# Kernel tuning notes

Hardware: AMD Instinct MI355X
Metric: run time of the kernel (lower is better)

The kernel has to match this reference:

```python
import jax, jax.numpy as jnp
import numpy as np

P = 32    # cardinality (number of parallel paths)
C = 256   # block input/output channels
D = 4     # bottleneck width per path
EPS = 1e-3  # Keras BatchNormalization default epsilon


def setup_inputs() -> dict:
    key = jax.random.key(0)
    ks = jax.random.split(key, 24)
    def nrm(k, shape, s=0.05):
        return jax.random.normal(k, shape, dtype=jnp.float32) * s
    inp = {}
    inp["x"] = jax.random.normal(ks[0], (8, 56, 56, C), dtype=jnp.float32)
    # conv weights/biases, stacked over the path axis P
    inp["W1"] = nrm(ks[1], (P, C, D))          # 1x1 conv C->4
    inp["B1"] = nrm(ks[2], (P, D))
    inp["W2"] = nrm(ks[3], (P, 3, 3, D, D))    # 3x3 conv 4->4 (HWIO)
    inp["B2"] = nrm(ks[4], (P, D))
    inp["W3"] = nrm(ks[5], (P, D, C))          # 1x1 conv 4->256
    inp["B3"] = nrm(ks[6], (P, C))
    # BatchNorm (inference): gamma, beta, moving mean, moving var per stage
    inp["G1"]  = 1.0 + nrm(ks[7], (P, D));  inp["Be1"] = nrm(ks[8], (P, D))
    inp["M1"]  = nrm(ks[9], (P, D));        inp["V1"]  = 1.0 + 0.1 * jax.random.uniform(ks[10], (P, D), dtype=jnp.float32)
    inp["G2"]  = 1.0 + nrm(ks[11], (P, D)); inp["Be2"] = nrm(ks[12], (P, D))
    inp["M2"]  = nrm(ks[13], (P, D));       inp["V2"]  = 1.0 + 0.1 * jax.random.uniform(ks[14], (P, D), dtype=jnp.float32)
    inp["G3"]  = 1.0 + nrm(ks[15], (P, C)); inp["Be3"] = nrm(ks[16], (P, C))
    inp["M3"]  = nrm(ks[17], (P, C));       inp["V3"]  = 1.0 + 0.1 * jax.random.uniform(ks[18], (P, C), dtype=jnp.float32)
    return inp


def _bn(x, g, b, m, v):
    # inference batch-norm: affine over channel axis
    return g * (x - m) * jax.lax.rsqrt(v + EPS) + b


def _path(x, w1, b1, g1, be1, m1, v1, w2, b2, g2, be2, m2, v2, w3, b3, g3, be3, m3, v3):
    h = jnp.einsum('nhwc,cd->nhwd', x, w1) + b1            # 1x1 conv C->D
    h = jax.nn.relu(_bn(h, g1, be1, m1, v1))
    h = jax.lax.conv_general_dilated(
        h, w2, window_strides=(1, 1), padding='SAME',
        dimension_numbers=('NHWC', 'HWIO', 'NHWC')) + b2   # 3x3 conv D->D
    h = jax.nn.relu(_bn(h, g2, be2, m2, v2))
    h = jnp.einsum('nhwd,dc->nhwc', h, w3) + b3            # 1x1 conv D->C
    h = jax.nn.relu(_bn(h, g3, be3, m3, v3))
    return h  # Dropout(0.2) is identity at inference


def reference(x, W1, B1, G1, Be1, M1, V1, W2, B2, G2, Be2, M2, V2, W3, B3, G3, Be3, M3, V3):
    # vmap over the 32 cardinality paths; x is shared (in_axes=None)
    paths = jax.vmap(_path, in_axes=(None,) + (0,) * 18)(
        x, W1, B1, G1, Be1, M1, V1, W2, B2, G2, Be2, M2, V2, W3, B3, G3, Be3, M3, V3)
    return jax.nn.relu(paths.sum(axis=0) + x)
```

## Files before the change

kernel.cpp:

```cpp
#include <hip/hip_runtime.h>

#define BATCH 8
#define HH 56
#define WW 56
#define NPOS (BATCH*HH*WW)
#define C 256
#define P 32
#define D 4
#define J 128
#define EPS 1e-3f
#define H2S 136

typedef __attribute__((ext_vector_type(8))) short bf16x8_t;
typedef __attribute__((ext_vector_type(4))) float f32x4_t;

__device__ __forceinline__ unsigned short f2bf(float f) {
    union { float f; unsigned int i; } v; v.f = f;
    unsigned int r = v.i + 0x7fffu + ((v.i >> 16) & 1u);
    return (unsigned short)(r >> 16);
}
__device__ __forceinline__ uint2 pack4_trunc(float4 v) {
    uint2 r;
    r.x = __builtin_amdgcn_perm(__float_as_uint(v.y), __float_as_uint(v.x), 0x07060302u);
    r.y = __builtin_amdgcn_perm(__float_as_uint(v.w), __float_as_uint(v.z), 0x07060302u);
    return r;
}

__global__ __launch_bounds__(256) void fold_params(
    const float* __restrict__ W1, const float* __restrict__ B1,
    const float* __restrict__ W2, const float* __restrict__ B2,
    const float* __restrict__ W3, const float* __restrict__ B3,
    const float* __restrict__ G1, const float* __restrict__ Be1,
    const float* __restrict__ M1, const float* __restrict__ V1,
    const float* __restrict__ G2, const float* __restrict__ Be2,
    const float* __restrict__ M2, const float* __restrict__ V2,
    const float* __restrict__ G3, const float* __restrict__ Be3,
    const float* __restrict__ M3, const float* __restrict__ V3,
    unsigned short* __restrict__ W1bf, float* __restrict__ b1f,
    float* __restrict__ w2q, float* __restrict__ b2t,
    unsigned short* __restrict__ WB, unsigned short* __restrict__ zb)
{
    int idx = blockIdx.x * 256 + threadIdx.x;

    if (idx < C*J) {
        int j = idx >> 8, c = idx & 255;
        int p = j >> 2, d = j & 3;
        float s = G1[j] * rsqrtf(V1[j] + EPS);
        W1bf[idx] = f2bf(W1[(p*C + c)*D + d] * s);
        return;
    }
    idx -= C*J;
    if (idx < J) {
        float s = G1[idx] * rsqrtf(V1[idx] + EPS);
        b1f[idx] = B1[idx] * s + Be1[idx] - M1[idx] * s;
        return;
    }
    idx -= J;
    if (idx < 9*D*D*P) {
        int do_ = idx & 3, p = (idx >> 2) & 31;
        int r2 = idx >> 7, di = r2 & 3, k9 = r2 >> 2;
        int j = p*4 + do_;
        float s = G2[j] * rsqrtf(V2[j] + EPS);
        w2q[idx] = W2[((p*9 + k9)*4 + di)*4 + do_] * s;
        return;
    }
    idx -= 9*D*D*P;
    if (idx < J) {
        int do_ = idx >> 5, p = idx & 31;
        int j = p*4 + do_;
        float s = G2[j] * rsqrtf(V2[j] + EPS);
        b2t[idx] = B2[j] * s + Be2[j] - M2[j] * s;
        return;
    }
    idx -= J;
    if (idx < P*C*8) {
        int s8 = idx & 7;
        int c = (idx >> 3) & 255;
        int p = idx >> 11;
        float sc = G3[p*C + c] * rsqrtf(V3[p*C + c] + EPS);
        float v = 0.f;
        if (s8 < 4)       v = W3[(p*D + s8)*C + c] * sc;
        else if (s8 == 4) v = B3[p*C + c] * sc + Be3[p*C + c] - M3[p*C + c] * sc;
        WB[idx] = f2bf(v);
        return;
    }
    idx -= P*C*8;
    if (idx < 8) { zb[idx] = 0; return; }
}

__global__ __launch_bounds__(256, 4) void fused_all(
    const float* __restrict__ x, const unsigned short* __restrict__ W1bf,
    const float* __restrict__ b1f, const float* __restrict__ w2q,
    const float* __restrict__ b2t, const unsigned short* __restrict__ WB,
    const unsigned short* __restrict__ zb, float* __restrict__ out)
{
    __shared__ unsigned short xs[36*256];
    __shared__ unsigned short h1L[36*132];
    __shared__ unsigned short h2s[16*H2S];

    const int tid = threadIdx.x;
    int bid = blockIdx.x;
    int wg = (bid & 7) * 196 + (bid >> 3);
    const int xb = wg % 14;  wg /= 14;
    const int yb = wg % 14;  const int b = wg / 14;
    const int wid = tid >> 6, l = tid & 63, l15 = l & 15, quad = l >> 4;
    const int j0w = wid * 32;

#pragma unroll
    for (int it = 0; it < 5; ++it) {
        int idx = it*256 + tid;
        int pos = idx >> 5, g = idx & 31;
        if (pos < 36) {
            int hy = (pos*43) >> 8, hx = pos - hy*6;
            int gy = yb*4 + hy - 1, gx = xb*4 + hx - 1;
            uint4 st; st.x = 0u; st.y = 0u; st.z = 0u; st.w = 0u;
            if (gy >= 0 && gy < HH && gx >= 0 && gx < WW) {
                const float* xp = &x[(size_t)((b*HH + gy)*WW + gx) * C + g*8];
                float4 v0 = *(const float4*)xp;
                float4 v1 = *(const float4*)(xp + 4);
                uint2 p0 = pack4_trunc(v0), p1 = pack4_trunc(v1);
                st.x = p0.x; st.y = p0.y; st.z = p1.x; st.w = p1.y;
            }
            *(uint4*)&xs[pos*256 + ((g ^ (pos & 7)) * 8)] = st;
        }
    }
    __syncthreads();

    union bu { uint4 u; bf16x8_t v; };
#pragma unroll
    for (int jf = 0; jf < 2; ++jf) {
        bu aw[8];
        const int wrow = j0w + jf*16 + l15;
#pragma unroll
        for (int kc = 0; kc < 8; ++kc)
            aw[kc].u = *(const uint4*)&W1bf[wrow*C + kc*32 + quad*8];
#pragma unroll
        for (int mt = 0; mt < 3; ++mt) {
            const int row = mt*16 + l15;
            const int rrow = (row < 36) ? row : 0;
            int hy = (row*43) >> 8;
            int hx = row - hy*6;
            int gy = yb*4 + hy - 1, gx = xb*4 + hx - 1;
            const bool valid = (row < 36) & (gy >= 0) & (gy < HH) & (gx >= 0) & (gx < WW);
            const unsigned mask = valid ? 0xFFFFFFFFu : 0u;
            f32x4_t acc = (f32x4_t){0.f,0.f,0.f,0.f};
#pragma unroll
            for (int kc = 0; kc < 8; ++kc) {
                int g = (kc*4 + quad) ^ (rrow & 7);
                bf16x8_t bb = *(const bf16x8_t*)&xs[rrow*256 + g*8];
                acc = __builtin_amdgcn_mfma_f32_16x16x32_bf16(aw[kc].v, bb, acc, 0, 0, 0);
            }
            if (row < 36) {
                int jb = j0w + jf*16 + quad*4;
                float4 bias = *(const float4*)&b1f[jb];
                float v0 = fmaxf(acc[0] + bias.x, 0.f);
                float v1 = fmaxf(acc[1] + bias.y, 0.f);
                float v2 = fmaxf(acc[2] + bias.z, 0.f);
                float v3 = fmaxf(acc[3] + bias.w, 0.f);
                uint2 o;
                o.x = ((unsigned int)f2bf(v0) | ((unsigned int)f2bf(v1) << 16)) & mask;
                o.y = ((unsigned int)f2bf(v2) | ((unsigned int)f2bf(v3) << 16)) & mask;
                *(uint2*)&h1L[row*132 + jb] = o;
            }
        }
    }

    const int pos = l15;
    const int py = pos >> 2, px = pos & 3;
#pragma unroll
    for (int i = 0; i < 2; ++i) {
        const int q = (l >> 4) * 2 + i;
        const int p = wid*8 + q;
        float a0 = b2t[p], a1 = b2t[32+p], a2 = b2t[64+p], a3 = b2t[96+p];
#pragma unroll
        for (int ky = 0; ky < 3; ++ky) {
#pragma unroll
            for (int kx = 0; kx < 3; ++kx) {
                const float* wp = &w2q[(ky*3 + kx) * 512 + p*4];
                float4 w0 = *(const float4*)&wp[0];
                float4 w1 = *(const float4*)&wp[128];
                float4 w2v = *(const float4*)&wp[256];
                float4 w3v = *(const float4*)&wp[384];
                int hp = (py + ky)*6 + px + kx;
                uint2 hv = *(const uint2*)&h1L[hp*132 + p*4];
                float f0 = __uint_as_float(hv.x << 16);
                float f1 = __uint_as_float(hv.x & 0xffff0000u);
                float f2 = __uint_as_float(hv.y << 16);
                float f3 = __uint_as_float(hv.y & 0xffff0000u);
                a0 = fmaf(f0, w0.x, a0);  a1 = fmaf(f0, w0.y, a1);
                a2 = fmaf(f0, w0.z, a2);  a3 = fmaf(f0, w0.w, a3);
                a0 = fmaf(f1, w1.x, a0);  a1 = fmaf(f1, w1.y, a1);
                a2 = fmaf(f1, w1.z, a2);  a3 = fmaf(f1, w1.w, a3);
                a0 = fmaf(f2, w2v.x, a0); a1 = fmaf(f2, w2v.y, a1);
                a2 = fmaf(f2, w2v.z, a2); a3 = fmaf(f2, w2v.w, a3);
                a0 = fmaf(f3, w3v.x, a0); a1 = fmaf(f3, w3v.y, a1);
                a2 = fmaf(f3, w3v.z, a2); a3 = fmaf(f3, w3v.w, a3);
            }
        }
        uint2 o;
        o.x = (unsigned int)f2bf(fmaxf(a0, 0.f)) |
              ((unsigned int)f2bf(fmaxf(a1, 0.f)) << 16);
        o.y = (unsigned int)f2bf(fmaxf(a2, 0.f)) |
              ((unsigned int)f2bf(fmaxf(a3, 0.f)) << 16);
        *(uint2*)&h2s[pos*H2S + p*4] = o;
    }
    __syncthreads();

    const int cb = wid * 64;
    const unsigned short* wbp;
    int pstr, cstr;
    if (quad == 0) {
        wbp = &WB[((size_t)(cb + l15)) * 8];
        pstr = C * 8;
        cstr = 16 * 8;
    } else {
        wbp = zb;
        pstr = 0; cstr = 0;
    }

    const f32x4_t zero = (f32x4_t){0.f, 0.f, 0.f, 0.f};
    f32x4_t dacc[4];
#pragma unroll
    for (int ct = 0; ct < 4; ++ct) dacc[ct] = zero;
    const unsigned int one = 0x3f80u;

#pragma unroll 2
    for (int pp = 0; pp < 16; ++pp) {
        uint4 h0 = *(const uint4*)&h2s[l15*H2S + pp*8];
        union au { unsigned int u[4]; bf16x8_t v; };
        au A0, A1;
        A0.u[0] = h0.x; A0.u[1] = h0.y; A0.u[2] = one; A0.u[3] = 0u;
        A1.u[0] = h0.z; A1.u[1] = h0.w; A1.u[2] = one; A1.u[3] = 0u;
        const unsigned short* pb0 = wbp + pp*2*pstr;
        const unsigned short* pb1 = pb0 + pstr;
#pragma unroll
        for (int ct = 0; ct < 4; ++ct) {
            union bu2 { uint4 u; bf16x8_t v; } B0, B1;
            B0.u = *(const uint4*)(pb0 + ct*cstr);
            B1.u = *(const uint4*)(pb1 + ct*cstr);
            f32x4_t z0 = __builtin_amdgcn_mfma_f32_16x16x32_bf16(A0.v, B0.v, zero, 0, 0, 0);
            f32x4_t z1 = __builtin_amdgcn_mfma_f32_16x16x32_bf16(A1.v, B1.v, zero, 0, 0, 0);
#pragma unroll
            for (int r = 0; r < 4; ++r)
                dacc[ct][r] += fmaxf(z0[r], 0.f) + fmaxf(z1[r], 0.f);
        }
    }

#pragma unroll
    for (int r = 0; r < 4; ++r) {
        int nl = quad*4 + r;
        int gy = yb*4 + (nl >> 2), gx = xb*4 + (nl & 3);
        size_t n = (size_t)((b*HH + gy)*WW + gx);
        const float* xr = &x[n*C + cb + l15];
        float* orow = &out[n*C + cb + l15];
#pragma unroll
        for (int ct = 0; ct < 4; ++ct) {
            float v = dacc[ct][r] + xr[ct*16];
            orow[ct*16] = fmaxf(v, 0.f);
        }
    }
}

extern "C" void kernel_launch(void* const* d_in, const int* in_sizes, int n_in,
                              void* d_out, int out_size, void* d_ws, size_t ws_size,
                              hipStream_t stream) {
    const float* x  = (const float*)d_in[0];
    const float* W1 = (const float*)d_in[1];
    const float* B1 = (const float*)d_in[2];
    const float* W2 = (const float*)d_in[3];
    const float* B2 = (const float*)d_in[4];
    const float* W3 = (const float*)d_in[5];
    const float* B3 = (const float*)d_in[6];
    const float* G1 = (const float*)d_in[7];
    const float* Be1= (const float*)d_in[8];
    const float* M1 = (const float*)d_in[9];
    const float* V1 = (const float*)d_in[10];
    const float* G2 = (const float*)d_in[11];
    const float* Be2= (const float*)d_in[12];
    const float* M2 = (const float*)d_in[13];
    const float* V2 = (const float*)d_in[14];
    const float* G3 = (const float*)d_in[15];
    const float* Be3= (const float*)d_in[16];
    const float* M3 = (const float*)d_in[17];
    const float* V3 = (const float*)d_in[18];

    char* wsb = (char*)d_ws;
    unsigned short* W1bf = (unsigned short*)(wsb + 0);
    unsigned short* WB   = (unsigned short*)(wsb + 65536);
    float*          w2q  = (float*)(wsb + 196608);
    float*          b1f  = (float*)(wsb + 215040);
    float*          b2t  = (float*)(wsb + 215552);
    unsigned short* zb   = (unsigned short*)(wsb + 216064);

    const int fold_tasks = C*J + J + 9*D*D*P + J + P*C*8 + 8;
    fold_params<<<(fold_tasks + 255)/256, 256, 0, stream>>>(
        W1, B1, W2, B2, W3, B3, G1, Be1, M1, V1, G2, Be2, M2, V2,
        G3, Be3, M3, V3, W1bf, b1f, w2q, b2t, WB, zb);

    fused_all<<<8*14*14, 256, 0, stream>>>(x, W1bf, b1f, w2q, b2t, WB, zb,
                                           (float*)d_out);
}
```

Measured before the change: 175.7 us.

## Stage 3x3 weights and biases in LDS and software-prefetch stage-3 B fragments

```diff
diff --git a/kernel.cpp b/kernel.cpp
--- a/kernel.cpp
+++ b/kernel.cpp
@@ -88,15 +88,16 @@
     if (idx < 8) { zb[idx] = 0; return; }
 }
 
-__global__ __launch_bounds__(256, 4) void fused_all(
+__global__ __launch_bounds__(256, 3) void fused_all(
     const float* __restrict__ x, const unsigned short* __restrict__ W1bf,
-    const float* __restrict__ b1f, const float* __restrict__ w2q,
-    const float* __restrict__ b2t, const unsigned short* __restrict__ WB,
+    const float* __restrict__ wsf,
+    const unsigned short* __restrict__ WB,
     const unsigned short* __restrict__ zb, float* __restrict__ out)
 {
     __shared__ unsigned short xs[36*256];
     __shared__ unsigned short h1L[36*132];
     __shared__ unsigned short h2s[16*H2S];
+    __shared__ float sw[4864];
 
     const int tid = threadIdx.x;
     int bid = blockIdx.x;
@@ -105,6 +106,15 @@
     const int yb = wg % 14;  const int b = wg / 14;
     const int wid = tid >> 6, l = tid & 63, l15 = l & 15, quad = l >> 4;
     const int j0w = wid * 32;
+
+#pragma unroll
+    for (int it = 0; it < 19; ++it) {
+        int i = it*256 + tid;
+        if (i < 4864) sw[i] = wsf[i];
+    }
+    const float* w2s = sw;
+    const float* b1s = sw + 4608;
+    const float* bs  = sw + 4736;
 
 #pragma unroll
     for (int it = 0; it < 5; ++it) {
@@ -152,7 +162,7 @@
             }
             if (row < 36) {
                 int jb = j0w + jf*16 + quad*4;
-                float4 bias = *(const float4*)&b1f[jb];
+                float4 bias = *(const float4*)&b1s[jb];
                 float v0 = fmaxf(acc[0] + bias.x, 0.f);
                 float v1 = fmaxf(acc[1] + bias.y, 0.f);
                 float v2 = fmaxf(acc[2] + bias.z, 0.f);
@@ -171,12 +181,12 @@
     for (int i = 0; i < 2; ++i) {
         const int q = (l >> 4) * 2 + i;
         const int p = wid*8 + q;
-        float a0 = b2t[p], a1 = b2t[32+p], a2 = b2t[64+p], a3 = b2t[96+p];
+        float a0 = bs[p], a1 = bs[32+p], a2 = bs[64+p], a3 = bs[96+p];
 #pragma unroll
         for (int ky = 0; ky < 3; ++ky) {
 #pragma unroll
             for (int kx = 0; kx < 3; ++kx) {
-                const float* wp = &w2q[(ky*3 + kx) * 512 + p*4];
+                const float* wp = &w2s[(ky*3 + kx) * 512 + p*4];
                 float4 w0 = *(const float4*)&wp[0];
                 float4 w1 = *(const float4*)&wp[128];
                 float4 w2v = *(const float4*)&wp[256];
@@ -224,22 +234,39 @@
     for (int ct = 0; ct < 4; ++ct) dacc[ct] = zero;
     const unsigned int one = 0x3f80u;
 
-#pragma unroll 2
+    union bu2 { uint4 u; bf16x8_t v; };
+    bu2 Ba[8], Bb[8];
+    uint4 ha, hb;
+#pragma unroll
+    for (int ct = 0; ct < 4; ++ct) {
+        Ba[2*ct].u   = *(const uint4*)(wbp + ct*cstr);
+        Ba[2*ct+1].u = *(const uint4*)(wbp + pstr + ct*cstr);
+    }
+    ha = *(const uint4*)&h2s[l15*H2S];
+
+#pragma unroll
     for (int pp = 0; pp < 16; ++pp) {
-        uint4 h0 = *(const uint4*)&h2s[l15*H2S + pp*8];
+        bu2* Bc = (pp & 1) ? Bb : Ba;
+        bu2* Bn = (pp & 1) ? Ba : Bb;
+        uint4 hc = (pp & 1) ? hb : ha;
+        if (pp < 15) {
+            const unsigned short* pbn = wbp + (size_t)(pp+1)*2*pstr;
+#pragma unroll
+            for (int ct = 0; ct < 4; ++ct) {
+                Bn[2*ct].u   = *(const uint4*)(pbn + ct*cstr);
+                Bn[2*ct+1].u = *(const uint4*)(pbn + pstr + ct*cstr);
+            }
+            uint4 hn = *(const uint4*)&h2s[l15*H2S + (pp+1)*8];
+            if (pp & 1) ha = hn; else hb = hn;
+        }
         union au { unsigned int u[4]; bf16x8_t v; };
         au A0, A1;
-        A0.u[0] = h0.x; A0.u[1] = h0.y; A0.u[2] = one; A0.u[3] = 0u;
-        A1.u[0] = h0.z; A1.u[1] = h0.w; A1.u[2] = one; A1.u[3] = 0u;
-        const unsigned short* pb0 = wbp + pp*2*pstr;
-        const unsigned short* pb1 = pb0 + pstr;
+        A0.u[0] = hc.x; A0.u[1] = hc.y; A0.u[2] = one; A0.u[3] = 0u;
+        A1.u[0] = hc.z; A1.u[1] = hc.w; A1.u[2] = one; A1.u[3] = 0u;
 #pragma unroll
         for (int ct = 0; ct < 4; ++ct) {
-            union bu2 { uint4 u; bf16x8_t v; } B0, B1;
-            B0.u = *(const uint4*)(pb0 + ct*cstr);
-            B1.u = *(const uint4*)(pb1 + ct*cstr);
-            f32x4_t z0 = __builtin_amdgcn_mfma_f32_16x16x32_bf16(A0.v, B0.v, zero, 0, 0, 0);
-            f32x4_t z1 = __builtin_amdgcn_mfma_f32_16x16x32_bf16(A1.v, B1.v, zero, 0, 0, 0);
+            f32x4_t z0 = __builtin_amdgcn_mfma_f32_16x16x32_bf16(A0.v, Bc[2*ct].v,   zero, 0, 0, 0);
+            f32x4_t z1 = __builtin_amdgcn_mfma_f32_16x16x32_bf16(A1.v, Bc[2*ct+1].v, zero, 0, 0, 0);
 #pragma unroll
             for (int r = 0; r < 4; ++r)
                 dacc[ct][r] += fmaxf(z0[r], 0.f) + fmaxf(z1[r], 0.f);
@@ -291,12 +318,13 @@
     float*          b1f  = (float*)(wsb + 215040);
     float*          b2t  = (float*)(wsb + 215552);
     unsigned short* zb   = (unsigned short*)(wsb + 216064);
+    const float*    wsf  = (const float*)(wsb + 196608);
 
     const int fold_tasks = C*J + J + 9*D*D*P + J + P*C*8 + 8;
     fold_params<<<(fold_tasks + 255)/256, 256, 0, stream>>>(
         W1, B1, W2, B2, W3, B3, G1, Be1, M1, V1, G2, Be2, M2, V2,
         G3, Be3, M3, V3, W1bf, b1f, w2q, b2t, WB, zb);
 
-    fused_all<<<8*14*14, 256, 0, stream>>>(x, W1bf, b1f, w2q, b2t, WB, zb,
+    fused_all<<<8*14*14, 256, 0, stream>>>(x, W1bf, wsf, WB, zb,
                                            (float*)d_out);
 }
```

After: 583.5 us. 232% more time.

## Compute grouped 3x3 conv with block-diagonal bf16 MFMA instead of scalar FMAs

Applied to the files above, without the earlier changes.

```diff
diff --git a/kernel.cpp b/kernel.cpp
--- a/kernel.cpp
+++ b/kernel.cpp
@@ -9,6 +9,7 @@
 #define D 4
 #define J 128
 #define EPS 1e-3f
+#define H1S 136
 #define H2S 136
 
 typedef __attribute__((ext_vector_type(8))) short bf16x8_t;
@@ -37,8 +38,9 @@
     const float* __restrict__ G3, const float* __restrict__ Be3,
     const float* __restrict__ M3, const float* __restrict__ V3,
     unsigned short* __restrict__ W1bf, float* __restrict__ b1f,
-    float* __restrict__ w2q, float* __restrict__ b2t,
-    unsigned short* __restrict__ WB, unsigned short* __restrict__ zb)
+    float* __restrict__ b2t,
+    unsigned short* __restrict__ WB, unsigned short* __restrict__ zb,
+    unsigned short* __restrict__ wbd)
 {
     int idx = blockIdx.x * 256 + threadIdx.x;
 
@@ -56,15 +58,6 @@
         return;
     }
     idx -= J;
-    if (idx < 9*D*D*P) {
-        int do_ = idx & 3, p = (idx >> 2) & 31;
-        int r2 = idx >> 7, di = r2 & 3, k9 = r2 >> 2;
-        int j = p*4 + do_;
-        float s = G2[j] * rsqrtf(V2[j] + EPS);
-        w2q[idx] = W2[((p*9 + k9)*4 + di)*4 + do_] * s;
-        return;
-    }
-    idx -= 9*D*D*P;
     if (idx < J) {
         int do_ = idx >> 5, p = idx & 31;
         int j = p*4 + do_;
@@ -86,17 +79,41 @@
     }
     idx -= P*C*8;
     if (idx < 8) { zb[idx] = 0; return; }
+    idx -= 8;
+    if (idx < 8*5*16*32) {
+        int k = idx & 31;
+        int rest = idx >> 5;
+        int n = rest & 15;
+        int rest2 = rest >> 4;
+        int tp = rest2 % 5;
+        int pg = rest2 / 5;
+        int tap = tp*2 + (k >> 4);
+        int pk = (k >> 2) & 3, di = k & 3;
+        int pn = n >> 2, do_ = n & 3;
+        float v = 0.f;
+        if (pk == pn && tap <= 8) {
+            int p = pg*4 + pn;
+            int j = p*4 + do_;
+            float s = G2[j] * rsqrtf(V2[j] + EPS);
+            v = W2[((p*9 + tap)*4 + di)*4 + do_] * s;
+        }
+        wbd[idx] = f2bf(v);
+        return;
+    }
 }
 
 __global__ __launch_bounds__(256, 4) void fused_all(
     const float* __restrict__ x, const unsigned short* __restrict__ W1bf,
-    const float* __restrict__ b1f, const float* __restrict__ w2q,
-    const float* __restrict__ b2t, const unsigned short* __restrict__ WB,
-    const unsigned short* __restrict__ zb, float* __restrict__ out)
+    const float* __restrict__ wsf,
+    const unsigned short* __restrict__ WB,
+    const unsigned short* __restrict__ zb,
+    const unsigned short* __restrict__ wbd,
+    float* __restrict__ out)
 {
     __shared__ unsigned short xs[36*256];
-    __shared__ unsigned short h1L[36*132];
+    __shared__ unsigned short h1L[36*H1S];
     __shared__ unsigned short h2s[16*H2S];
+    __shared__ float sw[256];
 
     const int tid = threadIdx.x;
     int bid = blockIdx.x;
@@ -105,6 +122,11 @@
     const int yb = wg % 14;  const int b = wg / 14;
     const int wid = tid >> 6, l = tid & 63, l15 = l & 15, quad = l >> 4;
     const int j0w = wid * 32;
+
+    if (tid < 256) {  }
+    if (tid < 256) sw[tid] = wsf[tid];
+    const float* b1s = sw;
+    const float* bs  = sw + 128;
 
 #pragma unroll
     for (int it = 0; it < 5; ++it) {
@@ -152,7 +174,7 @@
             }
             if (row < 36) {
                 int jb = j0w + jf*16 + quad*4;
-                float4 bias = *(const float4*)&b1f[jb];
+                float4 bias = *(const float4*)&b1s[jb];
                 float v0 = fmaxf(acc[0] + bias.x, 0.f);
                 float v1 = fmaxf(acc[1] + bias.y, 0.f);
                 float v2 = fmaxf(acc[2] + bias.z, 0.f);
@@ -160,49 +182,34 @@
                 uint2 o;
                 o.x = ((unsigned int)f2bf(v0) | ((unsigned int)f2bf(v1) << 16)) & mask;
                 o.y = ((unsigned int)f2bf(v2) | ((unsigned int)f2bf(v3) << 16)) & mask;
-                *(uint2*)&h1L[row*132 + jb] = o;
+                *(uint2*)&h1L[row*H1S + jb] = o;
             }
         }
     }
 
-    const int pos = l15;
-    const int py = pos >> 2, px = pos & 3;
-#pragma unroll
-    for (int i = 0; i < 2; ++i) {
-        const int q = (l >> 4) * 2 + i;
-        const int p = wid*8 + q;
-        float a0 = b2t[p], a1 = b2t[32+p], a2 = b2t[64+p], a3 = b2t[96+p];
-#pragma unroll
-        for (int ky = 0; ky < 3; ++ky) {
-#pragma unroll
-            for (int kx = 0; kx < 3; ++kx) {
-                const float* wp = &w2q[(ky*3 + kx) * 512 + p*4];
-                float4 w0 = *(const float4*)&wp[0];
-                float4 w1 = *(const float4*)&wp[128];
-                float4 w2v = *(const float4*)&wp[256];
-                float4 w3v = *(const float4*)&wp[384];
+    {
+        const int pos = l15, py = pos >> 2, px = pos & 3;
+#pragma unroll
+        for (int ig = 0; ig < 2; ++ig) {
+            const int pg = wid*2 + ig;
+            const int pD = pg*4 + (l15 >> 2), doD = l15 & 3;
+            const float bias = bs[doD*32 + pD];
+            f32x4_t cacc = (f32x4_t){bias, bias, bias, bias};
+#pragma unroll
+            for (int tp = 0; tp < 5; ++tp) {
+                int tap = tp*2 + (quad >> 1);
+                if (tap > 8) tap = 8;
+                int ky = (tap*11) >> 5;
+                int kx = tap - ky*3;
                 int hp = (py + ky)*6 + px + kx;
-                uint2 hv = *(const uint2*)&h1L[hp*132 + p*4];
-                float f0 = __uint_as_float(hv.x << 16);
-                float f1 = __uint_as_float(hv.x & 0xffff0000u);
-                float f2 = __uint_as_float(hv.y << 16);
-                float f3 = __uint_as_float(hv.y & 0xffff0000u);
-                a0 = fmaf(f0, w0.x, a0);  a1 = fmaf(f0, w0.y, a1);
-                a2 = fmaf(f0, w0.z, a2);  a3 = fmaf(f0, w0.w, a3);
-                a0 = fmaf(f1, w1.x, a0);  a1 = fmaf(f1, w1.y, a1);
-                a2 = fmaf(f1, w1.z, a2);  a3 = fmaf(f1, w1.w, a3);
-                a0 = fmaf(f2, w2v.x, a0); a1 = fmaf(f2, w2v.y, a1);
-                a2 = fmaf(f2, w2v.z, a2); a3 = fmaf(f2, w2v.w, a3);
-                a0 = fmaf(f3, w3v.x, a0); a1 = fmaf(f3, w3v.y, a1);
-                a2 = fmaf(f3, w3v.z, a2); a3 = fmaf(f3, w3v.w, a3);
+                bf16x8_t av = *(const bf16x8_t*)&h1L[hp*H1S + pg*16 + (quad & 1)*8];
+                bf16x8_t bv = *(const bf16x8_t*)&wbd[(((pg*5 + tp)*16 + l15) << 5) + quad*8];
+                cacc = __builtin_amdgcn_mfma_f32_16x16x32_bf16(av, bv, cacc, 0, 0, 0);
             }
-        }
-        uint2 o;
-        o.x = (unsigned int)f2bf(fmaxf(a0, 0.f)) |
-              ((unsigned int)f2bf(fmaxf(a1, 0.f)) << 16);
-        o.y = (unsigned int)f2bf(fmaxf(a2, 0.f)) |
-              ((unsigned int)f2bf(fmaxf(a3, 0.f)) << 16);
-        *(uint2*)&h2s[pos*H2S + p*4] = o;
+#pragma unroll
+            for (int r = 0; r < 4; ++r)
+                h2s[(quad*4 + r)*H2S + pg*16 + l15] = f2bf(fmaxf(cacc[r], 0.f));
+        }
     }
     __syncthreads();
 
@@ -287,16 +294,17 @@
     char* wsb = (char*)d_ws;
     unsigned short* W1bf = (unsigned short*)(wsb + 0);
     unsigned short* WB   = (unsigned short*)(wsb + 65536);
-    float*          w2q  = (float*)(wsb + 196608);
-    float*          b1f  = (float*)(wsb + 215040);
-    float*          b2t  = (float*)(wsb + 215552);
-    unsigned short* zb   = (unsigned short*)(wsb + 216064);
-
-    const int fold_tasks = C*J + J + 9*D*D*P + J + P*C*8 + 8;
+    float*          b1f  = (float*)(wsb + 196608);
+    float*          b2t  = (float*)(wsb + 197120);
+    unsigned short* zb   = (unsigned short*)(wsb + 197632);
+    unsigned short* wbd  = (unsigned short*)(wsb + 197648);
+    const float*    wsf  = (const float*)(wsb + 196608);
+
+    const int fold_tasks = C*J + J + J + P*C*8 + 8 + 8*5*16*32;
     fold_params<<<(fold_tasks + 255)/256, 256, 0, stream>>>(
         W1, B1, W2, B2, W3, B3, G1, Be1, M1, V1, G2, Be2, M2, V2,
-        G3, Be3, M3, V3, W1bf, b1f, w2q, b2t, WB, zb);
-
-    fused_all<<<8*14*14, 256, 0, stream>>>(x, W1bf, b1f, w2q, b2t, WB, zb,
+        G3, Be3, M3, V3, W1bf, b1f, b2t, WB, zb, wbd);
+
+    fused_all<<<8*14*14, 256, 0, stream>>>(x, W1bf, wsf, WB, zb, wbd,
                                            (float*)d_out);
 }
```

Result: faster. 167.5 us (-4.7%).
